# Kernel tuning notes

Measured on AMD Instinct MI355X. Metric: run time of the kernel, lower is better.

The kernel has to match this reference:

```python
import jax, jax.numpy as jnp
import numpy as np

N = 20000   # nodes
E = 320000  # edges
F0 = 32     # num_features
H = 8       # GAT heads
G = 64      # graphs in batch


def setup_inputs() -> dict:
    key = jax.random.key(0)
    ks = jax.random.split(key, 16)
    def p(k, shape, s=0.05):
        return jax.random.normal(k, shape, jnp.float32) * s
    d = {}
    d['x'] = jax.random.normal(ks[0], (N, F0), jnp.float32)
    d['edge_index'] = jax.random.randint(ks[1], (2, E), 0, N, dtype=jnp.int32)
    d['edge_weights'] = jax.random.uniform(ks[2], (E,), jnp.float32)
    d['batch'] = jnp.sort(jax.random.randint(ks[3], (N,), 0, G, dtype=jnp.int32))
    # GATConv(32 -> 32, heads=8)
    d['W_gat'] = p(ks[4], (F0, H * F0)); d['att_src'] = p(ks[5], (H, F0))
    d['att_dst'] = p(ks[6], (H, F0));    d['b_gat'] = jnp.zeros((H * F0,), jnp.float32)
    # residual Linear(256 -> 1024) (widened so the residual add is shape-consistent)
    d['W_res'] = p(ks[7], (H * F0, 1024)); d['b_res'] = jnp.zeros((1024,), jnp.float32)
    # GCNConv(256 -> 512) + BN1
    d['W2'] = p(ks[8], (H * F0, 512)); d['b2'] = jnp.zeros((512,), jnp.float32)
    d['g1'] = jnp.ones((512,), jnp.float32); d['be1'] = jnp.zeros((512,), jnp.float32)
    d['m1'] = jnp.zeros((512,), jnp.float32); d['v1'] = jnp.ones((512,), jnp.float32)
    # GCNConv(512 -> 1024) + BN2
    d['W3'] = p(ks[9], (512, 1024)); d['b3'] = jnp.zeros((1024,), jnp.float32)
    d['g2'] = jnp.ones((1024,), jnp.float32); d['be2'] = jnp.zeros((1024,), jnp.float32)
    d['m2'] = jnp.zeros((1024,), jnp.float32); d['v2'] = jnp.ones((1024,), jnp.float32)
    # head
    d['Wf1'] = p(ks[10], (1024, 256)); d['bf1'] = jnp.zeros((256,), jnp.float32)
    d['Wf2'] = p(ks[11], (256, 2));    d['bf2'] = jnp.zeros((2,), jnp.float32)
    return d


def _add_self_loops(edge_index, edge_weight, n):
    loop = jnp.arange(n, dtype=edge_index.dtype)
    ei = jnp.concatenate([edge_index, jnp.stack([loop, loop])], axis=1)
    ew = jnp.concatenate([edge_weight, jnp.ones((n,), edge_weight.dtype)])
    return ei, ew


def _gat(x, edge_index, W, att_src, att_dst, b, n):
    # PyG GATConv, concat=True, eval (attention dropout off). Self-loops already added.
    src, dst = edge_index[0], edge_index[1]
    h = (x @ W).reshape(n, H, -1)                    # [N,H,C]
    a_s = jnp.einsum('nhc,hc->nh', h, att_src)        # [N,H]
    a_d = jnp.einsum('nhc,hc->nh', h, att_dst)
    e = jax.nn.leaky_relu(a_s[src] + a_d[dst], 0.2)   # [E,H]
    m = jax.ops.segment_max(e, dst, num_segments=n)   # softmax over incoming edges
    ex = jnp.exp(e - m[dst])
    s = jax.ops.segment_sum(ex, dst, num_segments=n)
    alpha = ex / s[dst]
    out = jax.ops.segment_sum(h[src] * alpha[:, :, None], dst, num_segments=n)
    return out.reshape(n, -1) + b                     # [N,H*C]


def _gcn(x, edge_index, w, W, b, n):
    # PyG GCNConv with symmetric normalization; self-loops (weight 1) already added.
    src, dst = edge_index[0], edge_index[1]
    deg = jax.ops.segment_sum(w, dst, num_segments=n)
    dinv = jnp.where(deg > 0, jax.lax.rsqrt(jnp.maximum(deg, 1e-12)), 0.0)
    norm = dinv[src] * w * dinv[dst]                  # [E]
    h = x @ W                                         # transform first (cheaper)
    return jax.ops.segment_sum(h[src] * norm[:, None], dst, num_segments=n) + b


def _bn(x, g, b, m, v):
    return g * (x - m) * jax.lax.rsqrt(v + 1e-5) + b


def reference(x, edge_index, edge_weights, batch, W_gat, att_src, att_dst, b_gat,
              W_res, b_res, W2, b2, g1, be1, m1, v1, W3, b3, g2, be2, m2, v2,
              Wf1, bf1, Wf2, bf2):
    n = x.shape[0]
    ei, ew = _add_self_loops(edge_index, edge_weights, n)
    h = jax.nn.relu(_gat(x, ei, W_gat, att_src, att_dst, b_gat, n))   # [N,256]
    res = h @ W_res + b_res                                           # [N,1024]
    h = _gcn(h, ei, ew, W2, b2, n)                                    # [N,512]
    h = jax.nn.relu(_bn(h, g1, be1, m1, v1))
    h = _gcn(h, ei, ew, W3, b3, n)                                    # [N,1024]
    h = jax.nn.relu(_bn(h, g2, be2, m2, v2))
    h = h + res
    pooled = jax.ops.segment_max(h, batch, num_segments=G)            # global max pool [G,1024]
    z = jax.nn.relu(pooled @ Wf1 + bf1)                               # dropout is eval no-op
    return z @ Wf2 + bf2                                              # [G,2]
```

## Files before the change

kernel.cpp:

```cpp
#include <hip/hip_runtime.h>
#include <hip/hip_bf16.h>

#define NN 20000
#define EE 320000
#define GG 64
#define EN (EE + NN)
#define MT 157
#define SB 79

typedef float f32x4 __attribute__((ext_vector_type(4)));
typedef __bf16 bf16x4 __attribute__((ext_vector_type(4)));
typedef __bf16 bf16x8 __attribute__((ext_vector_type(8)));

__device__ __forceinline__ void gl_lds16(const void* g, void* l) {
    __builtin_amdgcn_global_load_lds((const __attribute__((address_space(1))) void*)g,
                                     (__attribute__((address_space(3))) void*)l, 16, 0, 0);
}

__global__ void sentinel_kernel(float* out, int n) {
    int i = blockIdx.x * 256 + threadIdx.x;
    if (i < n) out[i] = 12345.0f;
}

__global__ __launch_bounds__(256) void front_kernel(
    const float* __restrict__ W2, const float* __restrict__ W3, const float* __restrict__ Wres,
    __bf16* __restrict__ W2t, __bf16* __restrict__ W3t, __bf16* __restrict__ Wrt,
    const float* __restrict__ x, const float* __restrict__ W_gat,
    const float* __restrict__ att_s, const float* __restrict__ att_d,
    float* __restrict__ a_s, float* __restrict__ a_d,
    const int* __restrict__ ei, const float* __restrict__ ew,
    int* deg_cnt, float* deg_w, float* __restrict__ pooled)
{
    __shared__ float smemf[4160];
    int b = blockIdx.x, tid = threadIdx.x;
    if (b < 224) {
        const float* W; __bf16* Wt; int K, N, bx, by;
        if (b < 32)       { W = W2;   Wt = W2t; K = 256; N = 512;  int bb = b;       bx = bb & 7;  by = bb >> 3; }
        else if (b < 160) { W = W3;   Wt = W3t; K = 512; N = 1024; int bb = b - 32;  bx = bb & 15; by = bb >> 4; }
        else              { W = Wres; Wt = Wrt; K = 256; N = 1024; int bb = b - 160; bx = bb & 15; by = bb >> 4; }
        int kb = by * 64, nb = bx * 64;
        int tx = tid & 63, ty = tid >> 6;
#pragma unroll
        for (int i = ty; i < 64; i += 4)
            smemf[i * 65 + tx] = W[(size_t)(kb + i) * N + nb + tx];
        __syncthreads();
#pragma unroll
        for (int i = ty; i < 64; i += 4)
            Wt[(size_t)(nb + i) * K + kb + tx] = (__bf16)smemf[tx * 65 + i];
    } else if (b < 352) {
        int bb = b - 224;
        float* wss = smemf;
        float* wsd = smemf + 256;
        float* xs  = smemf + 512;
        {
            int h = tid >> 5, k = tid & 31;
            float s = 0.f, d = 0.f;
#pragma unroll
            for (int c = 0; c < 32; c++) {
                float wv = W_gat[k * 256 + h * 32 + c];
                s += wv * att_s[h * 32 + c];
                d += wv * att_d[h * 32 + c];
            }
            wss[h * 32 + k] = s; wsd[h * 32 + k] = d;
        }
        __syncthreads();
        for (int n0 = bb * 32; n0 < NN; n0 += 128 * 32) {
#pragma unroll
            for (int i = 0; i < 4; i++) {
                int idx = tid + i * 256;
                xs[(idx >> 5) * 33 + (idx & 31)] = x[(size_t)n0 * 32 + idx];
            }
            __syncthreads();
            int nl = tid >> 3, h = tid & 7;
            float s = 0.f, d = 0.f;
#pragma unroll
            for (int k = 0; k < 32; k++) {
                float xv = xs[nl * 33 + k];
                s += xv * wss[h * 32 + k];
                d += xv * wsd[h * 32 + k];
            }
            a_s[(n0 + nl) * 8 + h] = s;
            a_d[(n0 + nl) * 8 + h] = d;
            __syncthreads();
        }
    } else if (b < 608) {
        int i = (b - 352) * 256 + tid;
        pooled[i] = -INFINITY;
    } else {
        int e = (b - 608) * 256 + tid;
        if (e < EE) {
            int dst = ei[EE + e];
            atomicAdd(&deg_cnt[dst], 1);
            atomicAdd(&deg_w[dst], ew[e]);
        }
    }
}

__global__ __launch_bounds__(256) void scan_blocks(const int* __restrict__ deg_cnt, int* __restrict__ bsum) {
    __shared__ int red[256];
    int tid = threadIdx.x, i = blockIdx.x * 256 + tid;
    red[tid] = (i < NN) ? deg_cnt[i] + 1 : 0;
    __syncthreads();
    for (int s = 128; s > 0; s >>= 1) { if (tid < s) red[tid] += red[tid + s]; __syncthreads(); }
    if (tid == 0) bsum[blockIdx.x] = red[0];
}

__global__ __launch_bounds__(256) void scan_write(const int* __restrict__ deg_cnt,
                                                  const int* __restrict__ bsum, int* __restrict__ rowptr) {
    __shared__ int sc[256];
    __shared__ int red[256];
    int tid = threadIdx.x, b = blockIdx.x, i = b * 256 + tid;
    red[tid] = (tid < b && tid < SB) ? bsum[tid] : 0;
    __syncthreads();
    for (int s = 128; s > 0; s >>= 1) { if (tid < s) red[tid] += red[tid + s]; __syncthreads(); }
    int boff = red[0];
    __syncthreads();
    int v = (i < NN) ? deg_cnt[i] + 1 : 0;
    sc[tid] = v;
    __syncthreads();
    for (int ofs = 1; ofs < 256; ofs <<= 1) {
        int t = (tid >= ofs) ? sc[tid - ofs] : 0;
        __syncthreads();
        sc[tid] += t;
        __syncthreads();
    }
    if (i < NN) rowptr[i] = boff + sc[tid] - v;
    if (b == SB - 1 && tid == 255) rowptr[NN] = boff + sc[255];
}

__global__ void fill_kernel(const int* __restrict__ ei, const float* __restrict__ ew,
                            const float* __restrict__ deg_w, const int* __restrict__ rowptr,
                            int* fill, int2* __restrict__ csre) {
    int e = blockIdx.x * 256 + threadIdx.x;
    if (e >= EN) return;
    int src, dst; float w;
    if (e < EE) { src = ei[e]; dst = ei[EE + e]; w = ew[e]; }
    else        { src = dst = e - EE; w = 1.0f; }
    int pos = atomicAdd(&fill[dst], 1);
    int slot = rowptr[dst] + pos;
    float norm = rsqrtf(deg_w[src] + 1.0f) * w * rsqrtf(deg_w[dst] + 1.0f);
    csre[slot] = make_int2(src, __float_as_int(norm));
}


__global__ __launch_bounds__(256) void gat_agg_x(
    const int* __restrict__ rowptr, const int2* __restrict__ csre,
    const float* __restrict__ a_s, const float* __restrict__ a_d,
    const float* __restrict__ x, __bf16* __restrict__ xagg)
{
    int widx = threadIdx.x >> 6, lane = threadIdx.x & 63;
    int node = blockIdx.x * 4 + widx;
    int base = rowptr[node], deg = rowptr[node + 1] - base;
    int hA = lane & 7, eslot = lane >> 3;
    int c = lane & 31, half = lane >> 5;
    float adA = a_d[node * 8 + hA];
    float acc0[4] = {}, acc1[4] = {}, acc2[4] = {}, acc3[4] = {};

    if (deg <= 64) {
        int sv = (lane < deg) ? csre[base + lane].x : 0;
        float ev[8];
        float psum = 0.f;
#pragma unroll
        for (int j = 0; j < 8; j++) {
            int e = j * 8 + eslot;
            float v = 0.f;
            if (e < deg) {
                int src = __shfl(sv, e);
                float t = a_s[src * 8 + hA] + adA;
                t = (t > 0.f) ? t : 0.2f * t;
                v = __expf(t);
            }
            ev[j] = v;
            psum += v;
        }
#pragma unroll
        for (int m = 8; m <= 32; m <<= 1) psum += __shfl_xor(psum, m);
        float sinv[4];
#pragma unroll
        for (int jj = 0; jj < 4; jj++) sinv[jj] = 1.f / __shfl(psum, half * 4 + jj);
#pragma unroll
        for (int j = 0; j < 8; j++) {
            if (j * 8 >= deg) break;
            int lim = min(8, deg - j * 8);
            int t = 0;
            for (; t + 3 < lim; t += 4) {
                int sA = __shfl(sv, j * 8 + t),     sB = __shfl(sv, j * 8 + t + 1);
                int sC = __shfl(sv, j * 8 + t + 2), sD = __shfl(sv, j * 8 + t + 3);
                float xvA = x[(size_t)sA * 32 + c];
                float xvB = x[(size_t)sB * 32 + c];
                float xvC = x[(size_t)sC * 32 + c];
                float xvD = x[(size_t)sD * 32 + c];
#pragma unroll
                for (int jj = 0; jj < 4; jj++) {
                    int hb = half * 4 + jj;
                    acc0[jj] += __shfl(ev[j], (t << 3) | hb) * sinv[jj] * xvA;
                    acc1[jj] += __shfl(ev[j], ((t + 1) << 3) | hb) * sinv[jj] * xvB;
                    acc2[jj] += __shfl(ev[j], ((t + 2) << 3) | hb) * sinv[jj] * xvC;
                    acc3[jj] += __shfl(ev[j], ((t + 3) << 3) | hb) * sinv[jj] * xvD;
                }
            }
            for (; t < lim; t++) {
                int src = __shfl(sv, j * 8 + t);
                float xv = x[(size_t)src * 32 + c];
#pragma unroll
                for (int jj = 0; jj < 4; jj++) {
                    float a = __shfl(ev[j], (t << 3) | (half * 4 + jj)) * sinv[jj];
                    acc0[jj] += a * xv;
                }
            }
        }
    } else {
        float sum = 0.f;
        for (int e = 0; e < deg; e++) {
            int src = csre[base + e].x;
            float t = a_s[src * 8 + hA] + adA;
            t = (t > 0.f) ? t : 0.2f * t;
            sum += __expf(t);
        }
        float sinv[4], ad4[4];
#pragma unroll
        for (int jj = 0; jj < 4; jj++) {
            sinv[jj] = 1.f / __shfl(sum, half * 4 + jj);
            ad4[jj] = a_d[node * 8 + half * 4 + jj];
        }
        for (int e = 0; e < deg; e++) {
            int src = csre[base + e].x;
            float xv = x[(size_t)src * 32 + c];
#pragma unroll
            for (int jj = 0; jj < 4; jj++) {
                float t = a_s[src * 8 + half * 4 + jj] + ad4[jj];
                t = (t > 0.f) ? t : 0.2f * t;
                acc0[jj] += __expf(t) * sinv[jj] * xv;
            }
        }
    }
#pragma unroll
    for (int jj = 0; jj < 4; jj++)
        xagg[(size_t)node * 256 + (half * 4 + jj) * 32 + c] =
            (__bf16)((acc0[jj] + acc1[jj]) + (acc2[jj] + acc3[jj]));
}

__global__ __launch_bounds__(256) void gat_post(
    const __bf16* __restrict__ xagg, const float* __restrict__ W,
    const float* __restrict__ b_gat, __bf16* __restrict__ h1)
{
    __shared__ float Ws[32 * 256];
    int tid = threadIdx.x;
#pragma unroll
    for (int k = 0; k < 32; k++) Ws[k * 256 + tid] = W[k * 256 + tid];
    float bg = b_gat[tid];
    int lbase = tid & 32;
    __syncthreads();
    for (int n = blockIdx.x; n < NN; n += gridDim.x) {
        float xv = (float)xagg[(size_t)n * 256 + tid];
        float acc = 0.f;
#pragma unroll
        for (int k = 0; k < 32; k++) acc += __shfl(xv, lbase + k) * Ws[k * 256 + tid];
        h1[(size_t)n * 256 + tid] = (__bf16)fmaxf(acc + bg, 0.f);
    }
}

template <int C>
__global__ __launch_bounds__(256) void gcn_agg(
    const int* __restrict__ rowptr, const int2* __restrict__ csre,
    const __bf16* __restrict__ feat, __bf16* __restrict__ out)
{
    constexpr int V = C / 64;
    typedef __bf16 bf16v __attribute__((ext_vector_type(V)));
    int widx = threadIdx.x >> 6, lane = threadIdx.x & 63;
    int node = blockIdx.x * 4 + widx;
    int coff = lane * V;
    int base = rowptr[node], deg = rowptr[node + 1] - base;
    float acc0[V], acc1[V], acc2[V], acc3[V];
#pragma unroll
    for (int j = 0; j < V; j++) { acc0[j] = 0.f; acc1[j] = 0.f; acc2[j] = 0.f; acc3[j] = 0.f; }
    const __bf16* fb = feat + coff;
    for (int e0 = 0; e0 < deg; e0 += 64) {
        int cnt = min(64, deg - e0);
        int sv = 0; float wv = 0.f;
        if (lane < cnt) { int2 m = csre[base + e0 + lane]; sv = m.x; wv = __int_as_float(m.y); }
        int s = 0;
        for (; s + 7 < cnt; s += 8) {
            int si[8]; float wi[8];
#pragma unroll
            for (int u = 0; u < 8; u++) { si[u] = __shfl(sv, s + u); wi[u] = __shfl(wv, s + u); }
            bf16v f[8];
#pragma unroll
            for (int u = 0; u < 8; u++) f[u] = *(const bf16v*)(fb + (size_t)si[u] * C);
#pragma unroll
            for (int j = 0; j < V; j++) {
                acc0[j] += wi[0] * (float)f[0][j] + wi[4] * (float)f[4][j];
                acc1[j] += wi[1] * (float)f[1][j] + wi[5] * (float)f[5][j];
                acc2[j] += wi[2] * (float)f[2][j] + wi[6] * (float)f[6][j];
                acc3[j] += wi[3] * (float)f[3][j] + wi[7] * (float)f[7][j];
            }
        }
        for (; s + 3 < cnt; s += 4) {
            int sA = __shfl(sv, s),     sB = __shfl(sv, s + 1);
            int sC = __shfl(sv, s + 2), sD = __shfl(sv, s + 3);
            float wA = __shfl(wv, s),     wB = __shfl(wv, s + 1);
            float wC = __shfl(wv, s + 2), wD = __shfl(wv, s + 3);
            bf16v fA = *(const bf16v*)(fb + (size_t)sA * C);
            bf16v fB = *(const bf16v*)(fb + (size_t)sB * C);
            bf16v fC = *(const bf16v*)(fb + (size_t)sC * C);
            bf16v fD = *(const bf16v*)(fb + (size_t)sD * C);
#pragma unroll
            for (int j = 0; j < V; j++) {
                acc0[j] += wA * (float)fA[j]; acc1[j] += wB * (float)fB[j];
                acc2[j] += wC * (float)fC[j]; acc3[j] += wD * (float)fD[j];
            }
        }
        for (; s < cnt; s++) {
            int src = __shfl(sv, s);
            float w = __shfl(wv, s);
            bf16v f = *(const bf16v*)(fb + (size_t)src * C);
#pragma unroll
            for (int j = 0; j < V; j++) acc0[j] += w * (float)f[j];
        }
    }
    bf16v o;
#pragma unroll
    for (int j = 0; j < V; j++) o[j] = (__bf16)((acc0[j] + acc1[j]) + (acc2[j] + acc3[j]));
    *(bf16v*)(out + (size_t)node * C + coff) = o;
}


__device__ __forceinline__ void stage_async64(
    const __bf16* __restrict__ A, int K, const __bf16* __restrict__ Wt,
    int bm, int bn, int k0, int tid, __bf16* As, __bf16* Bs)
{
#pragma unroll
    for (int i = 0; i < 2; i++) {
        int j = i * 512 + tid;
        int r = j >> 3, c = j & 7;
        const __bf16* gp = A + (size_t)(bm + r) * K + k0 + ((c ^ (r & 7)) * 8);
        gl_lds16(gp, As + (size_t)(j & ~63) * 8);
    }
#pragma unroll
    for (int i = 0; i < 2; i++) {
        int j = i * 512 + tid;
        int r = j >> 3, c = j & 7;
        const __bf16* gp = Wt + (size_t)(bn + r) * K + k0 + ((c ^ (r & 7)) * 8);
        gl_lds16(gp, Bs + (size_t)(j & ~63) * 8);
    }
}

__device__ __forceinline__ void mfma_step64(
    const __bf16* As, const __bf16* Bs, int wr, int wc, int l16, int q, f32x4 (&acc)[4][2])
{
#pragma unroll
    for (int ks = 0; ks < 2; ks++) {
        bf16x8 af[4], bfv[2];
#pragma unroll
        for (int mt = 0; mt < 4; mt++) {
            int row = wr * 64 + mt * 16 + l16;
            af[mt] = *(const bf16x8*)(As + row * 64 + (((ks * 4 + q) ^ (row & 7)) * 8));
        }
#pragma unroll
        for (int nt = 0; nt < 2; nt++) {
            int row = wc * 32 + nt * 16 + l16;
            bfv[nt] = *(const bf16x8*)(Bs + row * 64 + (((ks * 4 + q) ^ (row & 7)) * 8));
        }
#pragma unroll
        for (int mt = 0; mt < 4; mt++)
#pragma unroll
            for (int nt = 0; nt < 2; nt++)
                acc[mt][nt] = __builtin_amdgcn_mfma_f32_16x16x32_bf16(af[mt], bfv[nt], acc[mt][nt], 0, 0, 0);
    }
}

__device__ __forceinline__ void gemm_loop(
    const __bf16* __restrict__ A, int K, const __bf16* __restrict__ Wt,
    int bm, int bn, int tid, int wr, int wc, int l16, int q,
    __bf16* As, __bf16* Bs, f32x4 (&acc)[4][2])
{
    for (int k0 = 0; k0 < K; k0 += 64) {
        stage_async64(A, K, Wt, bm, bn, k0, tid, As, Bs);
        __syncthreads();
        mfma_step64(As, Bs, wr, wc, l16, q, acc);
        __syncthreads();
    }
}

__global__ __launch_bounds__(512) void gemm_bn_relu(
    const __bf16* __restrict__ A, const __bf16* __restrict__ Wt,
    int M, int K, int Nc,
    const float* __restrict__ bias,
    const float* __restrict__ g, const float* __restrict__ be,
    const float* __restrict__ mu, const float* __restrict__ var,
    __bf16* __restrict__ C)
{
    __shared__ __bf16 As[128 * 64];
    __shared__ __bf16 Bs[128 * 64];
    int tid = threadIdx.x;
    int w = tid >> 6, wr = w >> 2, wc = w & 3;
    int l = tid & 63, q = l >> 4, l16 = l & 15;
    int i = blockIdx.x;
    int k = (i & 3) * MT + (i >> 2);
    int bm = (k >> 2) * 128, bn = (k & 3) * 128;
    f32x4 acc[4][2] = {};
    gemm_loop(A, K, Wt, bm, bn, tid, wr, wc, l16, q, As, Bs, acc);
#pragma unroll
    for (int nt = 0; nt < 2; nt++) {
        int gn = bn + wc * 32 + nt * 16 + l16;
        float s = g[gn] * rsqrtf(var[gn] + 1e-5f);
        float t = be[gn] - mu[gn] * s;
        float bv = bias[gn];
#pragma unroll
        for (int mt = 0; mt < 4; mt++)
#pragma unroll
            for (int r = 0; r < 4; r++) {
                int gm = bm + wr * 64 + mt * 16 + q * 4 + r;
                if (gm < M) C[(size_t)gm * Nc + gn] = (__bf16)fmaxf((acc[mt][nt][r] + bv) * s + t, 0.f);
            }
    }
}

__device__ __forceinline__ void atomicMaxFloat(float* addr, float value) {
    if (value >= 0.f) atomicMax((int*)addr, __float_as_int(value));
    else              atomicMin((unsigned int*)addr, __float_as_uint(value));
}

__global__ __launch_bounds__(512) void gemm_final(
    const __bf16* __restrict__ A1, const __bf16* __restrict__ W3t,
    const __bf16* __restrict__ A2, const __bf16* __restrict__ Wrt,
    const float* __restrict__ b3, const float* __restrict__ bres,
    const float* __restrict__ g, const float* __restrict__ be,
    const float* __restrict__ mu, const float* __restrict__ var,
    const int* __restrict__ batch, float* __restrict__ pooled)
{
    const int M = NN;
    __shared__ __bf16 As[128 * 64];
    __shared__ __bf16 Bs[128 * 64];
    __shared__ int bat[128];
    int tid = threadIdx.x;
    int w = tid >> 6, wr = w >> 2, wc = w & 3;
    int l = tid & 63, q = l >> 4, l16 = l & 15;
    int i = blockIdx.x;
    int k = (i & 7) * MT + (i >> 3);
    int bm = (k >> 3) * 128, bn = (k & 7) * 128;
    if (tid < 128) bat[tid] = (bm + tid < M) ? batch[bm + tid] : -1;
    f32x4 acc[4][2] = {};
    f32x4 accR[4][2] = {};
    gemm_loop(A1, 512, W3t, bm, bn, tid, wr, wc, l16, q, As, Bs, acc);
    gemm_loop(A2, 256, Wrt, bm, bn, tid, wr, wc, l16, q, As, Bs, accR);
#pragma unroll
    for (int nt = 0; nt < 2; nt++) {
        int gn = bn + wc * 32 + nt * 16 + l16;
        float s = g[gn] * rsqrtf(var[gn] + 1e-5f);
        float t = be[gn] - mu[gn] * s;
        float bv3 = b3[gn];
        float bvr = bres[gn];
        int cb = -1; float run = 0.f;
#pragma unroll
        for (int mt = 0; mt < 4; mt++)
#pragma unroll
            for (int r = 0; r < 4; r++) {
                int lr = wr * 64 + mt * 16 + q * 4 + r;
                int id = bat[lr];
                if (id < 0) continue;
                float v = fmaxf((acc[mt][nt][r] + bv3) * s + t, 0.f) + accR[mt][nt][r] + bvr;
                if (id == cb) run = fmaxf(run, v);
                else {
                    if (cb >= 0) atomicMaxFloat(&pooled[cb * 1024 + gn], run);
                    cb = id; run = v;
                }
            }
        if (cb >= 0) atomicMaxFloat(&pooled[cb * 1024 + gn], run);
    }
}

__global__ void head_kernel(
    const float* __restrict__ pooled, const float* __restrict__ Wf1, const float* __restrict__ bf1,
    const float* __restrict__ Wf2, const float* __restrict__ bf2, float* __restrict__ out)
{
    int gph = blockIdx.x, tid = threadIdx.x;
    __shared__ float prow[1024];
    __shared__ float zred[256];
    for (int i = tid; i < 1024; i += 256) prow[i] = pooled[gph * 1024 + i];
    __syncthreads();
    float z = 0.f;
    for (int k = 0; k < 1024; k++) z += prow[k] * Wf1[k * 256 + tid];
    z = fmaxf(z + bf1[tid], 0.f);
    for (int c = 0; c < 2; c++) {
        zred[tid] = z * Wf2[tid * 2 + c];
        __syncthreads();
        for (int s = 128; s > 0; s >>= 1) { if (tid < s) zred[tid] += zred[tid + s]; __syncthreads(); }
        if (tid == 0) out[gph * 2 + c] = zred[0] + bf2[c];
        __syncthreads();
    }
}

extern "C" void kernel_launch(void* const* d_in, const int* in_sizes, int n_in,
                              void* d_out, int out_size, void* d_ws, size_t ws_size,
                              hipStream_t stream) {
    const float* x       = (const float*)d_in[0];
    const int*   ei      = (const int*)d_in[1];
    const float* ew      = (const float*)d_in[2];
    const int*   batch   = (const int*)d_in[3];
    const float* W_gat   = (const float*)d_in[4];
    const float* att_src = (const float*)d_in[5];
    const float* att_dst = (const float*)d_in[6];
    const float* b_gat   = (const float*)d_in[7];
    const float* W_res   = (const float*)d_in[8];
    const float* b_res   = (const float*)d_in[9];
    const float* W2      = (const float*)d_in[10];
    const float* b2v     = (const float*)d_in[11];
    const float* g1      = (const float*)d_in[12];
    const float* be1     = (const float*)d_in[13];
    const float* m1      = (const float*)d_in[14];
    const float* v1      = (const float*)d_in[15];
    const float* W3      = (const float*)d_in[16];
    const float* b3      = (const float*)d_in[17];
    const float* g2      = (const float*)d_in[18];
    const float* be2     = (const float*)d_in[19];
    const float* m2      = (const float*)d_in[20];
    const float* v2      = (const float*)d_in[21];
    const float* Wf1     = (const float*)d_in[22];
    const float* bf1     = (const float*)d_in[23];
    const float* Wf2     = (const float*)d_in[24];
    const float* bf2v    = (const float*)d_in[25];
    float* out           = (float*)d_out;

    char* ws = (char*)d_ws;
    size_t off = 0;
    auto alloc = [&](size_t bytes) { size_t o = off; off += (bytes + 255) & ~(size_t)255; return o; };
    size_t o_hlin   = alloc((size_t)NN * 256 * 2);
    size_t o_h1     = alloc((size_t)NN * 256 * 2);
    size_t o_h2     = alloc((size_t)NN * 512 * 2);
    size_t o_agg2   = alloc((size_t)NN * 512 * 2);
    size_t o_as     = alloc((size_t)NN * 8 * 4);
    size_t o_ad     = alloc((size_t)NN * 8 * 4);
    size_t o_degc   = alloc((size_t)NN * 4);
    size_t o_degw   = alloc((size_t)NN * 4);
    size_t o_fill   = alloc((size_t)NN * 4);
    size_t o_rowptr = alloc((size_t)(NN + 1) * 4);
    size_t o_bsum   = alloc((size_t)SB * 4);
    size_t o_csre   = alloc((size_t)EN * 8);
    size_t o_pool   = alloc((size_t)GG * 1024 * 4);
    size_t o_w2t    = alloc((size_t)512 * 256 * 2);
    size_t o_w3t    = alloc((size_t)1024 * 512 * 2);
    size_t o_wrt    = alloc((size_t)1024 * 256 * 2);
    if (off > ws_size) {
        sentinel_kernel<<<(out_size + 255) / 256, 256, 0, stream>>>(out, out_size);
        return;
    }

    __bf16* xagg   = (__bf16*)(ws + o_hlin);
    __bf16* agg1   = xagg;
    __bf16* h1     = (__bf16*)(ws + o_h1);
    __bf16* h2     = (__bf16*)(ws + o_h2);
    __bf16* agg2   = (__bf16*)(ws + o_agg2);
    float*  a_s    = (float*)(ws + o_as);
    float*  a_d    = (float*)(ws + o_ad);
    int*    degc   = (int*)(ws + o_degc);
    float*  degw   = (float*)(ws + o_degw);
    int*    fillb  = (int*)(ws + o_fill);
    int*    rowptr = (int*)(ws + o_rowptr);
    int*    bsum   = (int*)(ws + o_bsum);
    int2*   csre   = (int2*)(ws + o_csre);
    float*  pooled = (float*)(ws + o_pool);
    __bf16* W2t    = (__bf16*)(ws + o_w2t);
    __bf16* W3t    = (__bf16*)(ws + o_w3t);
    __bf16* Wrt    = (__bf16*)(ws + o_wrt);

    hipMemsetAsync(ws + o_degc, 0, o_rowptr - o_degc, stream);
    front_kernel<<<1858, 256, 0, stream>>>(W2, W3, W_res, W2t, W3t, Wrt,
        x, W_gat, att_src, att_dst, a_s, a_d, ei, ew, degc, degw, pooled);

    scan_blocks<<<SB, 256, 0, stream>>>(degc, bsum);
    scan_write<<<SB, 256, 0, stream>>>(degc, bsum, rowptr);
    fill_kernel<<<(EN + 255) / 256, 256, 0, stream>>>(ei, ew, degw, rowptr, fillb, csre);

    gat_agg_x<<<NN / 4, 256, 0, stream>>>(rowptr, csre, a_s, a_d, x, xagg);
    gat_post<<<1280, 256, 0, stream>>>(xagg, W_gat, b_gat, h1);

    gcn_agg<256><<<NN / 4, 256, 0, stream>>>(rowptr, csre, h1, agg1);
    gemm_bn_relu<<<4 * MT, 512, 0, stream>>>(agg1, W2t, NN, 256, 512, b2v,
        g1, be1, m1, v1, h2);
    gcn_agg<512><<<NN / 4, 256, 0, stream>>>(rowptr, csre, h2, agg2);
    gemm_final<<<8 * MT, 512, 0, stream>>>(agg2, W3t, h1, Wrt,
        b3, b_res, g2, be2, m2, v2, batch, pooled);

    head_kernel<<<GG, 256, 0, stream>>>(pooled, Wf1, bf1, Wf2, bf2v, out);
}
```

Before: 411.2 us.

## Store layer-2 activations in FP8 and gather bf16 copy of x

The first BN+ReLU GEMM now writes its output as FP8 e4m3, scaled by 16. A new gcn_agg_fp8 kernel gathers these bytes and decodes them through a 256-entry LDS lookup table, which halves gather traffic for the 512-wide aggregation. The front kernel also converts x to bf16 so the GAT gather reads half as many bytes, and the 8-way unrolled path in gcn_agg is removed. The cost is precision: FP8 quantization of activations and bf16 rounding of x may affect accuracy tolerance.

```diff
diff --git a/kernel.cpp b/kernel.cpp
--- a/kernel.cpp
+++ b/kernel.cpp
@@ -1,5 +1,6 @@
 #include <hip/hip_runtime.h>
 #include <hip/hip_bf16.h>
+#include <hip/hip_fp8.h>
 
 #define NN 20000
 #define EE 320000
@@ -29,7 +30,8 @@
     const float* __restrict__ att_s, const float* __restrict__ att_d,
     float* __restrict__ a_s, float* __restrict__ a_d,
     const int* __restrict__ ei, const float* __restrict__ ew,
-    int* deg_cnt, float* deg_w, float* __restrict__ pooled)
+    int* deg_cnt, float* deg_w, float* __restrict__ pooled,
+    __bf16* __restrict__ xb)
 {
     __shared__ float smemf[4160];
     int b = blockIdx.x, tid = threadIdx.x;
@@ -86,12 +88,22 @@
     } else if (b < 608) {
         int i = (b - 352) * 256 + tid;
         pooled[i] = -INFINITY;
-    } else {
+    } else if (b < 1858) {
         int e = (b - 608) * 256 + tid;
         if (e < EE) {
             int dst = ei[EE + e];
             atomicAdd(&deg_cnt[dst], 1);
             atomicAdd(&deg_w[dst], ew[e]);
+        }
+    } else {
+        int idx0 = (b - 1858) * 2048 + tid * 8;
+        if (idx0 < NN * 32) {
+            f32x4 a = *(const f32x4*)(x + idx0);
+            f32x4 c = *(const f32x4*)(x + idx0 + 4);
+            bf16x8 o;
+#pragma unroll
+            for (int u = 0; u < 4; u++) { o[u] = (__bf16)a[u]; o[u + 4] = (__bf16)c[u]; }
+            *(bf16x8*)(xb + idx0) = o;
         }
     }
 }
@@ -142,11 +154,10 @@
     csre[slot] = make_int2(src, __float_as_int(norm));
 }
 
-
 __global__ __launch_bounds__(256) void gat_agg_x(
     const int* __restrict__ rowptr, const int2* __restrict__ csre,
     const float* __restrict__ a_s, const float* __restrict__ a_d,
-    const float* __restrict__ x, __bf16* __restrict__ xagg)
+    const __bf16* __restrict__ xb, __bf16* __restrict__ xagg)
 {
     int widx = threadIdx.x >> 6, lane = threadIdx.x & 63;
     int node = blockIdx.x * 4 + widx;
@@ -186,10 +197,10 @@
             for (; t + 3 < lim; t += 4) {
                 int sA = __shfl(sv, j * 8 + t),     sB = __shfl(sv, j * 8 + t + 1);
                 int sC = __shfl(sv, j * 8 + t + 2), sD = __shfl(sv, j * 8 + t + 3);
-                float xvA = x[(size_t)sA * 32 + c];
-                float xvB = x[(size_t)sB * 32 + c];
-                float xvC = x[(size_t)sC * 32 + c];
-                float xvD = x[(size_t)sD * 32 + c];
+                float xvA = (float)xb[(size_t)sA * 32 + c];
+                float xvB = (float)xb[(size_t)sB * 32 + c];
+                float xvC = (float)xb[(size_t)sC * 32 + c];
+                float xvD = (float)xb[(size_t)sD * 32 + c];
 #pragma unroll
                 for (int jj = 0; jj < 4; jj++) {
                     int hb = half * 4 + jj;
@@ -201,7 +212,7 @@
             }
             for (; t < lim; t++) {
                 int src = __shfl(sv, j * 8 + t);
-                float xv = x[(size_t)src * 32 + c];
+                float xv = (float)xb[(size_t)src * 32 + c];
 #pragma unroll
                 for (int jj = 0; jj < 4; jj++) {
                     float a = __shfl(ev[j], (t << 3) | (half * 4 + jj)) * sinv[jj];
@@ -225,7 +236,7 @@
         }
         for (int e = 0; e < deg; e++) {
             int src = csre[base + e].x;
-            float xv = x[(size_t)src * 32 + c];
+            float xv = (float)xb[(size_t)src * 32 + c];
 #pragma unroll
             for (int jj = 0; jj < 4; jj++) {
                 float t = a_s[src * 8 + half * 4 + jj] + ad4[jj];
@@ -280,21 +291,6 @@
         int sv = 0; float wv = 0.f;
         if (lane < cnt) { int2 m = csre[base + e0 + lane]; sv = m.x; wv = __int_as_float(m.y); }
         int s = 0;
-        for (; s + 7 < cnt; s += 8) {
-            int si[8]; float wi[8];
-#pragma unroll
-            for (int u = 0; u < 8; u++) { si[u] = __shfl(sv, s + u); wi[u] = __shfl(wv, s + u); }
-            bf16v f[8];
-#pragma unroll
-            for (int u = 0; u < 8; u++) f[u] = *(const bf16v*)(fb + (size_t)si[u] * C);
-#pragma unroll
-            for (int j = 0; j < V; j++) {
-                acc0[j] += wi[0] * (float)f[0][j] + wi[4] * (float)f[4][j];
-                acc1[j] += wi[1] * (float)f[1][j] + wi[5] * (float)f[5][j];
-                acc2[j] += wi[2] * (float)f[2][j] + wi[6] * (float)f[6][j];
-                acc3[j] += wi[3] * (float)f[3][j] + wi[7] * (float)f[7][j];
-            }
-        }
         for (; s + 3 < cnt; s += 4) {
             int sA = __shfl(sv, s),     sB = __shfl(sv, s + 1);
             int sC = __shfl(sv, s + 2), sD = __shfl(sv, s + 3);
@@ -324,6 +320,60 @@
     *(bf16v*)(out + (size_t)node * C + coff) = o;
 }
 
+__global__ __launch_bounds__(256) void gcn_agg_fp8(
+    const int* __restrict__ rowptr, const int2* __restrict__ csre,
+    const unsigned char* __restrict__ feat, __bf16* __restrict__ out)
+{
+    __shared__ float lut[256];
+    int tid = threadIdx.x;
+    {
+        unsigned char bb = (unsigned char)tid;
+        __hip_fp8_e4m3 q = *reinterpret_cast<__hip_fp8_e4m3*>(&bb);
+        lut[tid] = ((float)q) * 0.0625f;
+    }
+    __syncthreads();
+    int widx = tid >> 6, lane = tid & 63;
+    int node = blockIdx.x * 4 + widx;
+    int coff = lane * 8;
+    int base = rowptr[node], deg = rowptr[node + 1] - base;
+    float acc0[8] = {}, acc1[8] = {}, acc2[8] = {}, acc3[8] = {};
+    const unsigned char* fb = feat + coff;
+    for (int e0 = 0; e0 < deg; e0 += 64) {
+        int cnt = min(64, deg - e0);
+        int sv = 0; float wv = 0.f;
+        if (lane < cnt) { int2 m = csre[base + e0 + lane]; sv = m.x; wv = __int_as_float(m.y); }
+        int s = 0;
+        for (; s + 3 < cnt; s += 4) {
+            int sA = __shfl(sv, s),     sB = __shfl(sv, s + 1);
+            int sC = __shfl(sv, s + 2), sD = __shfl(sv, s + 3);
+            float wA = __shfl(wv, s),     wB = __shfl(wv, s + 1);
+            float wC = __shfl(wv, s + 2), wD = __shfl(wv, s + 3);
+            unsigned long long vA = *(const unsigned long long*)(fb + (size_t)sA * 512);
+            unsigned long long vB = *(const unsigned long long*)(fb + (size_t)sB * 512);
+            unsigned long long vC = *(const unsigned long long*)(fb + (size_t)sC * 512);
+            unsigned long long vD = *(const unsigned long long*)(fb + (size_t)sD * 512);
+#pragma unroll
+            for (int j = 0; j < 8; j++) {
+                acc0[j] += wA * lut[(vA >> (8 * j)) & 0xff];
+                acc1[j] += wB * lut[(vB >> (8 * j)) & 0xff];
+                acc2[j] += wC * lut[(vC >> (8 * j)) & 0xff];
+                acc3[j] += wD * lut[(vD >> (8 * j)) & 0xff];
+            }
+        }
+        for (; s < cnt; s++) {
+            int src = __shfl(sv, s);
+            float w = __shfl(wv, s);
+            unsigned long long v = *(const unsigned long long*)(fb + (size_t)src * 512);
+#pragma unroll
+            for (int j = 0; j < 8; j++) acc0[j] += w * lut[(v >> (8 * j)) & 0xff];
+        }
+    }
+    bf16x8 o;
+#pragma unroll
+    for (int j = 0; j < 8; j++) o[j] = (__bf16)((acc0[j] + acc1[j]) + (acc2[j] + acc3[j]));
+    *(bf16x8*)(out + (size_t)node * 512 + coff) = o;
+}
+
 
 __device__ __forceinline__ void stage_async64(
     const __bf16* __restrict__ A, int K, const __bf16* __restrict__ Wt,
@@ -388,7 +438,7 @@
     const float* __restrict__ bias,
     const float* __restrict__ g, const float* __restrict__ be,
     const float* __restrict__ mu, const float* __restrict__ var,
-    __bf16* __restrict__ C)
+    unsigned char* __restrict__ C)
 {
     __shared__ __bf16 As[128 * 64];
     __shared__ __bf16 Bs[128 * 64];
@@ -411,7 +461,11 @@
 #pragma unroll
             for (int r = 0; r < 4; r++) {
                 int gm = bm + wr * 64 + mt * 16 + q * 4 + r;
-                if (gm < M) C[(size_t)gm * Nc + gn] = (__bf16)fmaxf((acc[mt][nt][r] + bv) * s + t, 0.f);
+                if (gm < M) {
+                    float val = fmaxf((acc[mt][nt][r] + bv) * s + t, 0.f);
+                    *reinterpret_cast<__hip_fp8_e4m3*>(&C[(size_t)gm * Nc + gn]) =
+                        __hip_fp8_e4m3(16.0f * val);
+                }
             }
     }
 }
@@ -527,8 +581,9 @@
     auto alloc = [&](size_t bytes) { size_t o = off; off += (bytes + 255) & ~(size_t)255; return o; };
     size_t o_hlin   = alloc((size_t)NN * 256 * 2);
     size_t o_h1     = alloc((size_t)NN * 256 * 2);
-    size_t o_h2     = alloc((size_t)NN * 512 * 2);
+    size_t o_h2     = alloc((size_t)NN * 512);
     size_t o_agg2   = alloc((size_t)NN * 512 * 2);
+    size_t o_xb     = alloc((size_t)NN * 32 * 2);
     size_t o_as     = alloc((size_t)NN * 8 * 4);
     size_t o_ad     = alloc((size_t)NN * 8 * 4);
     size_t o_degc   = alloc((size_t)NN * 4);
@@ -549,8 +604,9 @@
     __bf16* xagg   = (__bf16*)(ws + o_hlin);
     __bf16* agg1   = xagg;
     __bf16* h1     = (__bf16*)(ws + o_h1);
-    __bf16* h2     = (__bf16*)(ws + o_h2);
+    unsigned char* h2f = (unsigned char*)(ws + o_h2);
     __bf16* agg2   = (__bf16*)(ws + o_agg2);
+    __bf16* xb     = (__bf16*)(ws + o_xb);
     float*  a_s    = (float*)(ws + o_as);
     float*  a_d    = (float*)(ws + o_ad);
     int*    degc   = (int*)(ws + o_degc);
@@ -565,20 +621,20 @@
     __bf16* Wrt    = (__bf16*)(ws + o_wrt);
 
     hipMemsetAsync(ws + o_degc, 0, o_rowptr - o_degc, stream);
-    front_kernel<<<1858, 256, 0, stream>>>(W2, W3, W_res, W2t, W3t, Wrt,
-        x, W_gat, att_src, att_dst, a_s, a_d, ei, ew, degc, degw, pooled);
+    front_kernel<<<2171, 256, 0, stream>>>(W2, W3, W_res, W2t, W3t, Wrt,
+        x, W_gat, att_src, att_dst, a_s, a_d, ei, ew, degc, degw, pooled, xb);
 
     scan_blocks<<<SB, 256, 0, stream>>>(degc, bsum);
     scan_write<<<SB, 256, 0, stream>>>(degc, bsum, rowptr);
     fill_kernel<<<(EN + 255) / 256, 256, 0, stream>>>(ei, ew, degw, rowptr, fillb, csre);
 
-    gat_agg_x<<<NN / 4, 256, 0, stream>>>(rowptr, csre, a_s, a_d, x, xagg);
+    gat_agg_x<<<NN / 4, 256, 0, stream>>>(rowptr, csre, a_s, a_d, xb, xagg);
     gat_post<<<1280, 256, 0, stream>>>(xagg, W_gat, b_gat, h1);
 
     gcn_agg<256><<<NN / 4, 256, 0, stream>>>(rowptr, csre, h1, agg1);
     gemm_bn_relu<<<4 * MT, 512, 0, stream>>>(agg1, W2t, NN, 256, 512, b2v,
-        g1, be1, m1, v1, h2);
-    gcn_agg<512><<<NN / 4, 256, 0, stream>>>(rowptr, csre, h2, agg2);
+        g1, be1, m1, v1, h2f);
+    gcn_agg_fp8<<<NN / 4, 256, 0, stream>>>(rowptr, csre, h2f, agg2);
     gemm_final<<<8 * MT, 512, 0, stream>>>(agg2, W3t, h1, Wrt,
         b3, b_res, g2, be2, m2, v2, batch, pooled);
 
```

Measured after the change: 381.6 us. 7.2% less time.
